# Kernel tuning notes

Hardware: AMD Instinct MI355X
Metric: run time of the kernel (lower is better)

The kernel has to match this reference:

```python
import jax, jax.numpy as jnp
import numpy as np

B, W, WIN_IN = 8, 2048, 1024
D, NH, DFF, L, KS = 512, 8, 2048, 4, 4
NGENES, G = 20000, 2048


def _ln(x, g, b, eps=1e-5):
    m = jnp.mean(x, -1, keepdims=True)
    v = jnp.var(x, -1, keepdims=True)
    return (x - m) * jax.lax.rsqrt(v + eps) * g + b


def _mha(q_in, kv_in, qkv_w, qkv_b, out_w, out_b, nh):
    d = q_in.shape[-1]
    hd = d // nh
    wq, wk, wv = qkv_w[:d], qkv_w[d:2 * d], qkv_w[2 * d:]
    bq, bk, bv = qkv_b[:d], qkv_b[d:2 * d], qkv_b[2 * d:]
    q = (q_in @ wq.T + bq).reshape(q_in.shape[0], q_in.shape[1], nh, hd)
    k = (kv_in @ wk.T + bk).reshape(kv_in.shape[0], kv_in.shape[1], nh, hd)
    v = (kv_in @ wv.T + bv).reshape(kv_in.shape[0], kv_in.shape[1], nh, hd)
    scores = jnp.einsum('bqhd,bkhd->bhqk', q, k) / jnp.sqrt(jnp.asarray(hd, q.dtype))
    a = jax.nn.softmax(scores, axis=-1)
    o = jnp.einsum('bhqk,bkhd->bqhd', a, v).reshape(q_in.shape[0], q_in.shape[1], d)
    return o @ out_w.T + out_b


def _posenc(S, d, dtype):
    pos = jnp.arange(S, dtype=jnp.float32)[:, None]
    div = jnp.exp(jnp.arange(0, d, 2, dtype=jnp.float32) * (-np.log(10000.0) / d))
    pe = jnp.zeros((S, d), jnp.float32)
    pe = pe.at[:, 0::2].set(jnp.sin(pos * div)).at[:, 1::2].set(jnp.cos(pos * div))
    return pe.astype(dtype)


def setup_inputs():
    key = jax.random.key(0)
    ks_ = jax.random.split(key, 12)

    def n(k, shape, s=0.02):
        return jax.random.normal(k, shape, jnp.float32) * s

    return dict(
        windows=jax.random.normal(ks_[0], (B, W, WIN_IN), jnp.float32),
        gene_ids=jax.random.randint(ks_[1], (G,), 0, NGENES),
        W_window=n(ks_[2], (D, WIN_IN)),
        enc_qkv_w=n(ks_[3], (L, 3 * D, D)),
        enc_qkv_b=jnp.zeros((L, 3 * D), jnp.float32),
        enc_out_w=n(ks_[4], (L, D, D)),
        enc_out_b=jnp.zeros((L, D), jnp.float32),
        enc_ln1_g=jnp.ones((L, D), jnp.float32),
        enc_ln1_b=jnp.zeros((L, D), jnp.float32),
        enc_ln2_g=jnp.ones((L, D), jnp.float32),
        enc_ln2_b=jnp.zeros((L, D), jnp.float32),
        enc_ff1_w=n(ks_[5], (L, DFF, D)),
        enc_ff1_b=jnp.zeros((L, DFF), jnp.float32),
        enc_ff2_w=n(ks_[6], (L, D, DFF)),
        enc_ff2_b=jnp.zeros((L, D), jnp.float32),
        gene_embed=n(ks_[7], (NGENES, D), 1.0),
        ca_qkv_w=n(ks_[8], (3 * D, D)),
        ca_qkv_b=jnp.zeros((3 * D,), jnp.float32),
        ca_out_w=n(ks_[9], (D, D)),
        ca_out_b=jnp.zeros((D,), jnp.float32),
        ro_ln_g=jnp.ones((D,), jnp.float32),
        ro_ln_b=jnp.zeros((D,), jnp.float32),
        ro_w=n(ks_[10], (1, D)),
        ro_b=jnp.zeros((1,), jnp.float32),
    )


def reference(windows, gene_ids, W_window, enc_qkv_w, enc_qkv_b, enc_out_w,
              enc_out_b, enc_ln1_g, enc_ln1_b, enc_ln2_g, enc_ln2_b,
              enc_ff1_w, enc_ff1_b, enc_ff2_w, enc_ff2_b, gene_embed,
              ca_qkv_w, ca_qkv_b, ca_out_w, ca_out_b, ro_ln_g, ro_ln_b,
              ro_w, ro_b):
    # proj_window (Linear, no bias; dropout inactive in eval)
    x = windows @ W_window.T                          # [B, W, D]
    Bn, Wn, _ = x.shape
    # AvgPool1d(kernel=stride=KS) along the window axis
    x = x.reshape(Bn, Wn // KS, KS, D).mean(axis=2)   # [B, S, D]
    S = x.shape[1]
    x = x + _posenc(S, D, x.dtype)[None]
    # pre-LN TransformerEncoder, relu FFN, no final norm
    for i in range(L):
        h = _ln(x, enc_ln1_g[i], enc_ln1_b[i])
        x = x + _mha(h, h, enc_qkv_w[i], enc_qkv_b[i], enc_out_w[i], enc_out_b[i], NH)
        h = _ln(x, enc_ln2_g[i], enc_ln2_b[i])
        x = x + (jax.nn.relu(h @ enc_ff1_w[i].T + enc_ff1_b[i]) @ enc_ff2_w[i].T + enc_ff2_b[i])
    # gene queries -> cross attention over encoded windows
    q = jnp.broadcast_to(gene_embed[gene_ids][None], (Bn, gene_ids.shape[0], D))
    z = _mha(q, x, ca_qkv_w, ca_qkv_b, ca_out_w, ca_out_b, NH)   # [B, G, D]
    pred = (_ln(z, ro_ln_g, ro_ln_b) @ ro_w.T + ro_b)[..., 0]    # [B, G]
    return pred, z
```

## Files before the change

### kernel.cpp

```cpp
#include <hip/hip_runtime.h>
#include <math.h>


typedef __attribute__((ext_vector_type(8))) short short8v;
typedef __attribute__((ext_vector_type(4))) float float4v;
typedef const __attribute__((address_space(1))) void* gas_t;
typedef __attribute__((address_space(3))) void* las_t;

__device__ inline unsigned short f2bf(float f) {
    unsigned int u = __builtin_bit_cast(unsigned int, f);
    return (unsigned short)((u + 0x7fffu + ((u >> 16) & 1u)) >> 16);
}

__device__ inline unsigned cvt_pk_bf16(float lo, float hi) {
    unsigned r;
    asm("v_cvt_pk_bf16_f32 %0, %1, %2" : "=v"(r) : "v"(lo), "v"(hi));
    return r;
}

__global__ __launch_bounds__(256) void cvt_k(const float* __restrict__ src,
                                             unsigned short* __restrict__ dst, int n4)
{
    int i = blockIdx.x * 256 + threadIdx.x;
    if (i >= n4) return;
    float4 v = ((const float4*)src)[i];
    ushort4 o;
    o.x = f2bf(v.x); o.y = f2bf(v.y); o.z = f2bf(v.z); o.w = f2bf(v.w);
    ((ushort4*)dst)[i] = o;
}

__global__ __launch_bounds__(256) void pool_windows_k(const float* __restrict__ win,
                                                      unsigned short* __restrict__ pw)
{
    int idx = blockIdx.x * 256 + threadIdx.x;
    int n = idx >> 8, c4 = (idx & 255) << 2;
    const float* base = win + (size_t)n * 4096 + c4;
    float4 a = *(const float4*)(base);
    float4 b2 = *(const float4*)(base + 1024);
    float4 c = *(const float4*)(base + 2048);
    float4 d = *(const float4*)(base + 3072);
    ushort4 r;
    r.x = f2bf((a.x + b2.x + c.x + d.x) * 0.25f);
    r.y = f2bf((a.y + b2.y + c.y + d.y) * 0.25f);
    r.z = f2bf((a.z + b2.z + c.z + d.z) * 0.25f);
    r.w = f2bf((a.w + b2.w + c.w + d.w) * 0.25f);
    ((ushort4*)pw)[idx] = r;
}

template<int BM, bool BIAS, bool BROW, bool RES, bool RELU, bool POSENC, bool O32, bool O16>
__global__ __launch_bounds__(256) void gemm_bf16_k(
    const unsigned short* __restrict__ A, const unsigned short* __restrict__ Bw,
    const float* __restrict__ bias, const float* __restrict__ Res,
    float* __restrict__ C32, unsigned short* __restrict__ C16,
    int M, int N, int K)
{
    constexpr int WC   = (BM == 128) ? 2 : 4;
    constexpr int NSTEP = 128 / WC;
    constexpr int MFR  = 4;
    constexpr int NFR  = NSTEP / 16;
    __shared__ __align__(16) unsigned short As[2][BM * 32];
    __shared__ __align__(16) unsigned short Bs[2][128 * 32];
    const int tid = threadIdx.x;
    const int lane = tid & 63;
    const int m0 = blockIdx.x * BM, n0 = blockIdx.y * 128;
    const int wr = (BM == 128) ? (tid >> 7) : 0;
    const int wc = (tid >> 6) & (WC - 1);
    const unsigned short* gA0 = A + (size_t)(m0 + (tid >> 2)) * K + (tid & 3) * 8;
    const unsigned short* gA1 = A + (size_t)(m0 + (tid >> 2) + 64) * K + (tid & 3) * 8;
    const unsigned short* gB0 = Bw + (size_t)(n0 + (tid >> 2)) * K + (tid & 3) * 8;
    const unsigned short* gB1 = Bw + (size_t)(n0 + (tid >> 2) + 64) * K + (tid & 3) * 8;
    const int r = lane & 15, g = lane >> 4;
    const int aoff = (64 * wr + r) * 32 + g * 8;
    const int boff = (NSTEP * wc + r) * 32 + g * 8;

    auto stage = [&](int bi, int k0) {
        __builtin_amdgcn_global_load_lds((gas_t)(gA0 + k0), (las_t)(&As[bi][tid * 8]), 16, 0, 0);
        if constexpr (BM == 128)
            __builtin_amdgcn_global_load_lds((gas_t)(gA1 + k0), (las_t)(&As[bi][(tid + 256) * 8]), 16, 0, 0);
        __builtin_amdgcn_global_load_lds((gas_t)(gB0 + k0), (las_t)(&Bs[bi][tid * 8]), 16, 0, 0);
        __builtin_amdgcn_global_load_lds((gas_t)(gB1 + k0), (las_t)(&Bs[bi][(tid + 256) * 8]), 16, 0, 0);
    };

    float4v acc[MFR][NFR];
    float4v z4 = {0.f, 0.f, 0.f, 0.f};
    #pragma unroll
    for (int i = 0; i < MFR; ++i)
        #pragma unroll
        for (int j = 0; j < NFR; ++j) acc[i][j] = z4;

    stage(0, 0);
    int buf = 0;
    for (int k0 = 0; k0 < K; k0 += 32) {
        __syncthreads();
        if (k0 + 32 < K) stage(buf ^ 1, k0 + 32);
        short8v a[MFR], b[NFR];
        #pragma unroll
        for (int mi = 0; mi < MFR; ++mi) a[mi] = *(const short8v*)&As[buf][aoff + mi * (16 * 32)];
        #pragma unroll
        for (int ni = 0; ni < NFR; ++ni) b[ni] = *(const short8v*)&Bs[buf][boff + ni * (16 * 32)];
        #pragma unroll
        for (int mi = 0; mi < MFR; ++mi)
            #pragma unroll
            for (int ni = 0; ni < NFR; ++ni)
                acc[mi][ni] = __builtin_amdgcn_mfma_f32_16x16x32_bf16(a[mi], b[ni], acc[mi][ni], 0, 0, 0);
        buf ^= 1;
    }

    #pragma unroll
    for (int mi = 0; mi < MFR; ++mi) {
        #pragma unroll
        for (int ni = 0; ni < NFR; ++ni) {
            const int row0 = m0 + 64 * wr + 16 * mi + g * 4;
            const int col  = n0 + NSTEP * wc + 16 * ni + r;
            float bv = (BIAS && !BROW) ? bias[col] : 0.f;
            float fr = 0.f;
            if (POSENC) fr = __expf((float)(col & ~1) * -0.01798894600f);
            #pragma unroll
            for (int q = 0; q < 4; ++q) {
                const int row = row0 + q;
                float v = acc[mi][ni][q] + bv;
                if (BIAS && BROW) v += bias[row];
                if (POSENC) {
                    float ang = (float)(row & 511) * fr;
                    v += (col & 1) ? __cosf(ang) : __sinf(ang);
                }
                if (RES) v += Res[(size_t)row * N + col];
                if (RELU) v = fmaxf(v, 0.0f);
                if (O32) C32[(size_t)row * N + col] = v;
                if (O16) C16[(size_t)row * N + col] = f2bf(v);
            }
        }
    }
}

template<bool SPLIT>
__global__ __launch_bounds__(256) void flashc_k(
    const unsigned short* __restrict__ Qp, long long q_bs, int q_rs,
    const unsigned short* __restrict__ Kp, long long k_bs, int k_rs,
    const unsigned short* __restrict__ Vtp, long long v_hs, long long v_bs, int v_rs,
    unsigned short* __restrict__ Op, long long o_bs, int o_rs,
    unsigned short* __restrict__ opart, float2* __restrict__ Ml,
    int nsplit, int nc)
{
    constexpr float C1 = 0.18033688011112042f;
    __shared__ __align__(16) unsigned short Kb[2][64 * 64];
    __shared__ __align__(16) unsigned short Vb[2][64 * 64];
    __shared__ __align__(16) unsigned short Ps[64 * 64];
    const int qt = blockIdx.x, h = blockIdx.y, z = blockIdx.z;
    const int b = z / nsplit, s = z - b * nsplit;
    const unsigned short* Q  = Qp  + (size_t)b * q_bs + (size_t)h * 64;
    const unsigned short* Kg = Kp  + (size_t)b * k_bs + (size_t)h * 64 + (size_t)(s * nc * 64) * k_rs;
    const unsigned short* Vg = Vtp + (size_t)h * v_hs + (size_t)b * v_bs + (size_t)(s * nc) * 64;
    const int q0 = qt * 64;
    const int tid = threadIdx.x, lane = tid & 63, w = tid >> 6;
    const int r = lane & 15, g = lane >> 4;
    const int sw8 = (r & 7) * 8;
    const int cA = (g * 8) ^ sw8;
    const int cB = ((g + 4) * 8) ^ sw8;
    const int prow = (16 * w + r) * 64;

    const unsigned short* qrow = Q + (size_t)(q0 + 16 * w + r) * q_rs + g * 8;
    short8v qf0 = *(const short8v*)(qrow);
    short8v qf1 = *(const short8v*)(qrow + 32);

    const int r0 = tid >> 3, cc = tid & 7;
    const int srcc = (cc ^ (r0 & 7)) * 8;
    auto stage = [&](int bi, int c) {
        const unsigned short* kc_ = Kg + (size_t)c * 64 * k_rs;
        const unsigned short* vc_ = Vg + (size_t)c * 64;
        __builtin_amdgcn_global_load_lds((gas_t)(kc_ + (size_t)r0 * k_rs + srcc),
                                         (las_t)(&Kb[bi][tid * 8]), 16, 0, 0);
        __builtin_amdgcn_global_load_lds((gas_t)(kc_ + (size_t)(r0 + 32) * k_rs + srcc),
                                         (las_t)(&Kb[bi][(tid + 256) * 8]), 16, 0, 0);
        __builtin_amdgcn_global_load_lds((gas_t)(vc_ + (size_t)r0 * v_rs + srcc),
                                         (las_t)(&Vb[bi][tid * 8]), 16, 0, 0);
        __builtin_amdgcn_global_load_lds((gas_t)(vc_ + (size_t)(r0 + 32) * v_rs + srcc),
                                         (las_t)(&Vb[bi][(tid + 256) * 8]), 16, 0, 0);
    };

    float4v acc_o[4];
    float4v z4 = {0.f, 0.f, 0.f, 0.f};
    #pragma unroll
    for (int dt = 0; dt < 4; ++dt) acc_o[dt] = z4;
    float m_own = -INFINITY, l_own = 0.f;

    stage(0, 0);
    __syncthreads();
    int buf = 0;

    for (int c = 0; c < nc; ++c) {
        if (c + 1 < nc) stage(buf ^ 1, c + 1);
        const unsigned short* KL = Kb[buf];
        const unsigned short* VL = Vb[buf];

        __builtin_amdgcn_s_setprio(1);
        float4v accs[4];
        #pragma unroll
        for (int t = 0; t < 4; ++t) {
            accs[t] = z4;
            const unsigned short* krow = KL + (16 * t + r) * 64;
            short8v kf0 = *(const short8v*)(krow + cA);
            short8v kf1 = *(const short8v*)(krow + cB);
            accs[t] = __builtin_amdgcn_mfma_f32_16x16x32_bf16(kf0, qf0, accs[t], 0, 0, 0);
            accs[t] = __builtin_amdgcn_mfma_f32_16x16x32_bf16(kf1, qf1, accs[t], 0, 0, 0);
        }
        __builtin_amdgcn_s_setprio(0);

        float m0_ = fmaxf(fmaxf(accs[0][0], accs[0][1]), fmaxf(accs[0][2], accs[0][3]));
        float m1_ = fmaxf(fmaxf(accs[1][0], accs[1][1]), fmaxf(accs[1][2], accs[1][3]));
        float m2_ = fmaxf(fmaxf(accs[2][0], accs[2][1]), fmaxf(accs[2][2], accs[2][3]));
        float m3_ = fmaxf(fmaxf(accs[3][0], accs[3][1]), fmaxf(accs[3][2], accs[3][3]));
        float sm = fmaxf(fmaxf(m0_, m1_), fmaxf(m2_, m3_));
        sm = fmaxf(sm, __shfl_xor(sm, 16));
        sm = fmaxf(sm, __shfl_xor(sm, 32));

        if (__any(sm > m_own + 64.f)) {
            float mn = fmaxf(m_own, sm);
            float alpha = __builtin_amdgcn_exp2f((m_own - mn) * C1);
            m_own = mn;
            float a0_ = __shfl(alpha, g * 4 + 0);
            float a1_ = __shfl(alpha, g * 4 + 1);
            float a2_ = __shfl(alpha, g * 4 + 2);
            float a3_ = __shfl(alpha, g * 4 + 3);
            #pragma unroll
            for (int dt = 0; dt < 4; ++dt) {
                acc_o[dt][0] *= a0_; acc_o[dt][1] *= a1_;
                acc_o[dt][2] *= a2_; acc_o[dt][3] *= a3_;
            }
            l_own *= alpha;
        }

        const float m2c = m_own * C1;
        float p[4][4];
        float rsum = 0.f;
        #pragma unroll
        for (int t = 0; t < 4; ++t)
            #pragma unroll
            for (int j = 0; j < 4; ++j) {
                float pv = __builtin_amdgcn_exp2f(__builtin_fmaf(accs[t][j], C1, -m2c));
                p[t][j] = pv; rsum += pv;
            }
        rsum += __shfl_xor(rsum, 16);
        rsum += __shfl_xor(rsum, 32);
        l_own += rsum;

        #pragma unroll
        for (int t = 0; t < 4; ++t) {
            uint2 uu;
            uu.x = cvt_pk_bf16(p[t][0], p[t][1]);
            uu.y = cvt_pk_bf16(p[t][2], p[t][3]);
            int pc = (((2 * t + (g >> 1)) * 8) ^ sw8) + (g & 1) * 4;
            *(uint2*)&Ps[prow + pc] = uu;
        }

        __builtin_amdgcn_s_setprio(1);
        short8v pf0 = *(const short8v*)&Ps[prow + cA];
        short8v pf1 = *(const short8v*)&Ps[prow + cB];
        #pragma unroll
        for (int dt = 0; dt < 4; ++dt) {
            const unsigned short* vrow = VL + (16 * dt + r) * 64;
            short8v vf0 = *(const short8v*)(vrow + cA);
            short8v vf1 = *(const short8v*)(vrow + cB);
            acc_o[dt] = __builtin_amdgcn_mfma_f32_16x16x32_bf16(pf0, vf0, acc_o[dt], 0, 0, 0);
            acc_o[dt] = __builtin_amdgcn_mfma_f32_16x16x32_bf16(pf1, vf1, acc_o[dt], 0, 0, 0);
        }
        __builtin_amdgcn_s_setprio(0);

        __syncthreads();
        buf ^= 1;
    }

    float il0 = 1.f / __shfl(l_own, g * 4 + 0);
    float il1 = 1.f / __shfl(l_own, g * 4 + 1);
    float il2 = 1.f / __shfl(l_own, g * 4 + 2);
    float il3 = 1.f / __shfl(l_own, g * 4 + 3);
    if (SPLIT) {
        unsigned short* Ob = opart + ((size_t)(s * 4096 + b * 512)) * 512 + h * 64;
        #pragma unroll
        for (int dt = 0; dt < 4; ++dt) {
            Ob[(size_t)(q0 + 16 * w + g * 4 + 0) * 512 + 16 * dt + r] = f2bf(acc_o[dt][0] * il0);
            Ob[(size_t)(q0 + 16 * w + g * 4 + 1) * 512 + 16 * dt + r] = f2bf(acc_o[dt][1] * il1);
            Ob[(size_t)(q0 + 16 * w + g * 4 + 2) * 512 + 16 * dt + r] = f2bf(acc_o[dt][2] * il2);
            Ob[(size_t)(q0 + 16 * w + g * 4 + 3) * 512 + 16 * dt + r] = f2bf(acc_o[dt][3] * il3);
        }
        if (g == 0)
            Ml[((size_t)(s * 8 + b) * 8 + h) * 512 + q0 + 16 * w + r] = make_float2(m_own, l_own);
    } else {
        unsigned short* O = Op + (size_t)b * o_bs + (size_t)h * 64;
        #pragma unroll
        for (int dt = 0; dt < 4; ++dt) {
            O[(size_t)(q0 + 16 * w + g * 4 + 0) * o_rs + 16 * dt + r] = f2bf(acc_o[dt][0] * il0);
            O[(size_t)(q0 + 16 * w + g * 4 + 1) * o_rs + 16 * dt + r] = f2bf(acc_o[dt][1] * il1);
            O[(size_t)(q0 + 16 * w + g * 4 + 2) * o_rs + 16 * dt + r] = f2bf(acc_o[dt][2] * il2);
            O[(size_t)(q0 + 16 * w + g * 4 + 3) * o_rs + 16 * dt + r] = f2bf(acc_o[dt][3] * il3);
        }
    }
}

template<int NS>
__global__ __launch_bounds__(256) void combine_k(const unsigned short* __restrict__ opart,
                                                 const float2* __restrict__ Ml,
                                                 unsigned short* __restrict__ Oo)
{
    constexpr float C1 = 0.18033688011112042f;
    const int row = blockIdx.x;
    const int b = row >> 9, srow = row & 511;
    const int tid = threadIdx.x;
    const int h = tid >> 5, t = tid & 31;
    float2 ml[NS];
    float m = -INFINITY;
    #pragma unroll
    for (int s = 0; s < NS; ++s) {
        ml[s] = Ml[((size_t)(s * 8 + b) * 8 + h) * 512 + srow];
        m = fmaxf(m, ml[s].x);
    }
    float wgt[NS];
    float wsum = 0.f;
    #pragma unroll
    for (int s = 0; s < NS; ++s) {
        wgt[s] = __builtin_amdgcn_exp2f((ml[s].x - m) * C1) * ml[s].y;
        wsum += wgt[s];
    }
    float inv = 1.f / wsum;
    const int col = h * 64 + t * 2;
    float acc0 = 0.f, acc1 = 0.f;
    #pragma unroll
    for (int s = 0; s < NS; ++s) {
        unsigned u = *(const unsigned*)&opart[((size_t)s * 4096 + row) * 512 + col];
        acc0 += wgt[s] * __builtin_bit_cast(float, (u & 0xffffu) << 16);
        acc1 += wgt[s] * __builtin_bit_cast(float, (u >> 16) << 16);
    }
    *(unsigned*)&Oo[(size_t)row * 512 + col] = cvt_pk_bf16(acc0 * inv, acc1 * inv);
}

__global__ __launch_bounds__(64) void ln_k(const float* __restrict__ X, unsigned short* __restrict__ Y,
                                           const float* __restrict__ g, const float* __restrict__ bt)
{
    int row = blockIdx.x, lane = threadIdx.x;
    const float* x = X + (size_t)row * 512;
    int c0 = lane * 4, c1 = 256 + lane * 4;
    float4 a0 = *(const float4*)&x[c0];
    float4 a1 = *(const float4*)&x[c1];
    float s  = a0.x + a0.y + a0.z + a0.w + a1.x + a1.y + a1.z + a1.w;
    float ss = a0.x * a0.x + a0.y * a0.y + a0.z * a0.z + a0.w * a0.w
             + a1.x * a1.x + a1.y * a1.y + a1.z * a1.z + a1.w * a1.w;
    #pragma unroll
    for (int off = 1; off < 64; off <<= 1) { s += __shfl_xor(s, off); ss += __shfl_xor(ss, off); }
    float mean = s * (1.f / 512.f);
    float var  = ss * (1.f / 512.f) - mean * mean;
    float rs = rsqrtf(var + 1e-5f);
    float4 g0 = *(const float4*)&g[c0], g1 = *(const float4*)&g[c1];
    float4 b0 = *(const float4*)&bt[c0], b1 = *(const float4*)&bt[c1];
    unsigned short* y = Y + (size_t)row * 512;
    ushort4 o0, o1;
    o0.x = f2bf((a0.x - mean) * rs * g0.x + b0.x);  o0.y = f2bf((a0.y - mean) * rs * g0.y + b0.y);
    o0.z = f2bf((a0.z - mean) * rs * g0.z + b0.z);  o0.w = f2bf((a0.w - mean) * rs * g0.w + b0.w);
    o1.x = f2bf((a1.x - mean) * rs * g1.x + b1.x);  o1.y = f2bf((a1.y - mean) * rs * g1.y + b1.y);
    o1.z = f2bf((a1.z - mean) * rs * g1.z + b1.z);  o1.w = f2bf((a1.w - mean) * rs * g1.w + b1.w);
    *(ushort4*)&y[c0] = o0;
    *(ushort4*)&y[c1] = o1;
}

__global__ __launch_bounds__(128) void gather_k(const float* __restrict__ ge, const int* __restrict__ ids,
                                                unsigned short* __restrict__ out)
{
    int gi = blockIdx.x, t = threadIdx.x;
    int id = ids[gi];
    float4 v = *(const float4*)&ge[(size_t)id * 512 + t * 4];
    ushort4 o;
    o.x = f2bf(v.x); o.y = f2bf(v.y); o.z = f2bf(v.z); o.w = f2bf(v.w);
    *(ushort4*)&out[(size_t)gi * 512 + t * 4] = o;
}

__global__ __launch_bounds__(64) void readout_k(const float* __restrict__ Z,
                                                const float* __restrict__ g, const float* __restrict__ bt,
                                                const float* __restrict__ rw, const float* __restrict__ rb,
                                                float* __restrict__ pred)
{
    int row = blockIdx.x, lane = threadIdx.x;
    const float* zr = Z + (size_t)row * 512;
    int c0 = lane * 4, c1 = 256 + lane * 4;
    float4 a0 = *(const float4*)&zr[c0];
    float4 a1 = *(const float4*)&zr[c1];
    float s  = a0.x + a0.y + a0.z + a0.w + a1.x + a1.y + a1.z + a1.w;
    float ss = a0.x * a0.x + a0.y * a0.y + a0.z * a0.z + a0.w * a0.w
             + a1.x * a1.x + a1.y * a1.y + a1.z * a1.z + a1.w * a1.w;
    #pragma unroll
    for (int off = 1; off < 64; off <<= 1) { s += __shfl_xor(s, off); ss += __shfl_xor(ss, off); }
    float mean = s * (1.f / 512.f);
    float var  = ss * (1.f / 512.f) - mean * mean;
    float rs = rsqrtf(var + 1e-5f);
    float4 g0 = *(const float4*)&g[c0], g1 = *(const float4*)&g[c1];
    float4 b0 = *(const float4*)&bt[c0], b1 = *(const float4*)&bt[c1];
    float4 w0 = *(const float4*)&rw[c0], w1 = *(const float4*)&rw[c1];
    float acc = 0.f;
    acc += ((a0.x - mean) * rs * g0.x + b0.x) * w0.x;
    acc += ((a0.y - mean) * rs * g0.y + b0.y) * w0.y;
    acc += ((a0.z - mean) * rs * g0.z + b0.z) * w0.z;
    acc += ((a0.w - mean) * rs * g0.w + b0.w) * w0.w;
    acc += ((a1.x - mean) * rs * g1.x + b1.x) * w1.x;
    acc += ((a1.y - mean) * rs * g1.y + b1.y) * w1.y;
    acc += ((a1.z - mean) * rs * g1.z + b1.z) * w1.z;
    acc += ((a1.w - mean) * rs * g1.w + b1.w) * w1.w;
    #pragma unroll
    for (int off = 1; off < 64; off <<= 1) acc += __shfl_xor(acc, off);
    if (lane == 0) pred[row] = acc + rb[0];
}

extern "C" void kernel_launch(void* const* d_in, const int* in_sizes, int n_in,
                              void* d_out, int out_size, void* d_ws, size_t ws_size,
                              hipStream_t stream)
{
    (void)in_sizes; (void)n_in; (void)out_size; (void)ws_size;
    const float* windows    = (const float*)d_in[0];
    const int*   gene_ids   = (const int*)  d_in[1];
    const float* W_window   = (const float*)d_in[2];
    const float* enc_qkv_w  = (const float*)d_in[3];
    const float* enc_qkv_b  = (const float*)d_in[4];
    const float* enc_out_w  = (const float*)d_in[5];
    const float* enc_out_b  = (const float*)d_in[6];
    const float* enc_ln1_g  = (const float*)d_in[7];
    const float* enc_ln1_b  = (const float*)d_in[8];
    const float* enc_ln2_g  = (const float*)d_in[9];
    const float* enc_ln2_b  = (const float*)d_in[10];
    const float* enc_ff1_w  = (const float*)d_in[11];
    const float* enc_ff1_b  = (const float*)d_in[12];
    const float* enc_ff2_w  = (const float*)d_in[13];
    const float* enc_ff2_b  = (const float*)d_in[14];
    const float* gene_embed = (const float*)d_in[15];
    const float* ca_qkv_w   = (const float*)d_in[16];
    const float* ca_qkv_b   = (const float*)d_in[17];
    const float* ca_out_w   = (const float*)d_in[18];
    const float* ca_out_b   = (const float*)d_in[19];
    const float* ro_ln_g    = (const float*)d_in[20];
    const float* ro_ln_b    = (const float*)d_in[21];
    const float* ro_w       = (const float*)d_in[22];
    const float* ro_b       = (const float*)d_in[23];

    float* pred = (float*)d_out;
    float* z    = pred + (size_t)8 * 2048;

    char* wp = (char*)d_ws;
    float* x = (float*)wp;                       wp += (size_t)4096 * 512 * 4;
    unsigned short* x16   = (unsigned short*)wp; wp += (size_t)4096 * 512 * 2;
    unsigned short* h16   = (unsigned short*)wp; wp += (size_t)4096 * 512 * 2;
    unsigned short* qkv16 = (unsigned short*)wp; wp += (size_t)4096 * 1536 * 2;
    unsigned short* ao16  = (unsigned short*)wp; wp += (size_t)4096 * 512 * 2;
    unsigned short* big16 = (unsigned short*)wp; wp += (size_t)16384 * 512 * 2;
    unsigned short* vt16  = (unsigned short*)wp; wp += (size_t)512 * 4096 * 2;
    unsigned short* wW16     = (unsigned short*)wp; wp += (size_t)512 * 1024 * 2;
    unsigned short* wqkv16   = (unsigned short*)wp; wp += (size_t)4 * 1536 * 512 * 2;
    unsigned short* wout16   = (unsigned short*)wp; wp += (size_t)4 * 512 * 512 * 2;
    unsigned short* wff116   = (unsigned short*)wp; wp += (size_t)4 * 2048 * 512 * 2;
    unsigned short* wff216   = (unsigned short*)wp; wp += (size_t)4 * 512 * 2048 * 2;
    unsigned short* wcaqkv16 = (unsigned short*)wp; wp += (size_t)1536 * 512 * 2;
    unsigned short* wcaout16 = (unsigned short*)wp; wp += (size_t)512 * 512 * 2;
    unsigned short* pw16    = big16;
    unsigned short* ff116   = big16;
    unsigned short* oc16    = big16;
    unsigned short* opart16 = big16;
    float2* mlbuf = (float2*)(big16 + (size_t)2 * 4096 * 512);
    unsigned short* ge16  = qkv16;
    unsigned short* qg16  = qkv16 + (size_t)2048 * 512;
    unsigned short* kc16  = qkv16 + (size_t)2 * 2048 * 512;

    auto cvt = [&](const float* s, unsigned short* d, int n) {
        cvt_k<<<(n / 4 + 255) / 256, 256, 0, stream>>>(s, d, n / 4);
    };
    cvt(W_window,  wW16,     512 * 1024);
    cvt(enc_qkv_w, wqkv16,   4 * 1536 * 512);
    cvt(enc_out_w, wout16,   4 * 512 * 512);
    cvt(enc_ff1_w, wff116,   4 * 2048 * 512);
    cvt(enc_ff2_w, wff216,   4 * 512 * 2048);
    cvt(ca_qkv_w,  wcaqkv16, 1536 * 512);
    cvt(ca_out_w,  wcaout16, 512 * 512);

    pool_windows_k<<<4096, 256, 0, stream>>>(windows, pw16);
    gemm_bf16_k<64, false, false, false, false, true, true, false><<<dim3(64, 4), 256, 0, stream>>>(
        pw16, wW16, nullptr, nullptr, x, nullptr, 4096, 512, 1024);

    for (int l = 0; l < 4; ++l) {
        const unsigned short* wl = wqkv16 + (size_t)l * 1536 * 512;
        ln_k<<<4096, 64, 0, stream>>>(x, h16, enc_ln1_g + l * 512, enc_ln1_b + l * 512);
        gemm_bf16_k<128, true, false, false, false, false, false, true><<<dim3(32, 8), 256, 0, stream>>>(
            h16, wl, enc_qkv_b + l * 1536, nullptr, nullptr, qkv16, 4096, 1024, 512);
        gemm_bf16_k<64, true, true, false, false, false, false, true><<<dim3(8, 32), 256, 0, stream>>>(
            wl + (size_t)1024 * 512, h16, enc_qkv_b + l * 1536 + 1024, nullptr,
            nullptr, vt16, 512, 4096, 512);
        flashc_k<true><<<dim3(8, 8, 16), 256, 0, stream>>>(
            qkv16, (long long)512 * 1024, 1024,
            qkv16 + 512, (long long)512 * 1024, 1024,
            vt16, (long long)64 * 4096, 512LL, 4096,
            nullptr, 0LL, 0,
            opart16, mlbuf, 2, 4);
        combine_k<2><<<4096, 256, 0, stream>>>(opart16, mlbuf, ao16);
        gemm_bf16_k<64, true, false, true, false, false, true, false><<<dim3(64, 4), 256, 0, stream>>>(
            ao16, wout16 + (size_t)l * 512 * 512, enc_out_b + l * 512, x, x, nullptr, 4096, 512, 512);
        ln_k<<<4096, 64, 0, stream>>>(x, h16, enc_ln2_g + l * 512, enc_ln2_b + l * 512);
        gemm_bf16_k<128, true, false, false, true, false, false, true><<<dim3(32, 16), 256, 0, stream>>>(
            h16, wff116 + (size_t)l * 2048 * 512, enc_ff1_b + l * 2048, nullptr,
            nullptr, ff116, 4096, 2048, 512);
        if (l == 3)
            gemm_bf16_k<64, true, false, true, false, false, true, true><<<dim3(64, 4), 256, 0, stream>>>(
                ff116, wff216 + (size_t)l * 512 * 2048, enc_ff2_b + l * 512, x, x, x16, 4096, 512, 2048);
        else
            gemm_bf16_k<64, true, false, true, false, false, true, false><<<dim3(64, 4), 256, 0, stream>>>(
                ff116, wff216 + (size_t)l * 512 * 2048, enc_ff2_b + l * 512, x, x, nullptr, 4096, 512, 2048);
    }

    gather_k<<<2048, 128, 0, stream>>>(gene_embed, gene_ids, ge16);
    gemm_bf16_k<64, true, false, false, false, false, false, true><<<dim3(32, 4), 256, 0, stream>>>(
        ge16, wcaqkv16, ca_qkv_b, nullptr, nullptr, qg16, 2048, 512, 512);
    gemm_bf16_k<64, true, false, false, false, false, false, true><<<dim3(64, 4), 256, 0, stream>>>(
        x16, wcaqkv16 + (size_t)512 * 512, ca_qkv_b + 512, nullptr, nullptr, kc16, 4096, 512, 512);
    gemm_bf16_k<64, true, true, false, false, false, false, true><<<dim3(8, 32), 256, 0, stream>>>(
        wcaqkv16 + (size_t)1024 * 512, x16, ca_qkv_b + 1024, nullptr, nullptr, vt16, 512, 4096, 512);
    flashc_k<false><<<dim3(32, 8, 8), 256, 0, stream>>>(
        qg16, 0LL, 512,
        kc16, (long long)512 * 512, 512,
        vt16, (long long)64 * 4096, 512LL, 4096,
        oc16, (long long)2048 * 512, 512,
        nullptr, nullptr, 1, 8);
    gemm_bf16_k<128, true, false, false, false, false, true, false><<<dim3(128, 4), 256, 0, stream>>>(
        oc16, wcaout16, ca_out_b, nullptr, z, nullptr, 16384, 512, 512);

    readout_k<<<16384, 64, 0, stream>>>(z, ro_ln_g, ro_ln_b, ro_w, ro_b, pred);
}
```

Before: 602.2 us.

## Deepen GEMM K-tile, XOR-swizzle LDS, and overlap loads with explicit vmcnt waits

The GEMM main loop is restructured. BM=64 tiles now use a 64-wide K slice, LDS columns are XOR-swizzled to avoid bank conflicts, and the single __syncthreads is replaced by explicit s_waitcnt vmcnt plus raw s_barrier, so the next stage's global-to-LDS loads stay in flight across the barrier. This is meant to cut barrier and LDS conflict stalls and improve load/compute overlap. In exchange, BM=64 uses more LDS and the code depends on the hand-counted vmcnt matching the number of outstanding loads.

```diff
diff --git a/kernel.cpp b/kernel.cpp
--- a/kernel.cpp
+++ b/kernel.cpp
@@ -54,31 +54,44 @@
     float* __restrict__ C32, unsigned short* __restrict__ C16,
     int M, int N, int K)
 {
+    constexpr int BK   = (BM == 128) ? 32 : 64;
+    constexpr int CPR  = BK / 8;
     constexpr int WC   = (BM == 128) ? 2 : 4;
     constexpr int NSTEP = 128 / WC;
     constexpr int MFR  = 4;
     constexpr int NFR  = NSTEP / 16;
-    __shared__ __align__(16) unsigned short As[2][BM * 32];
-    __shared__ __align__(16) unsigned short Bs[2][128 * 32];
+    constexpr int LPTA = BM * BK / 2048;
+    constexpr int LPTB = 128 * BK / 2048;
+    constexpr int LPT  = LPTA + LPTB;
+    __shared__ __align__(16) unsigned short As[2][BM * BK];
+    __shared__ __align__(16) unsigned short Bs[2][128 * BK];
     const int tid = threadIdx.x;
     const int lane = tid & 63;
     const int m0 = blockIdx.x * BM, n0 = blockIdx.y * 128;
     const int wr = (BM == 128) ? (tid >> 7) : 0;
     const int wc = (tid >> 6) & (WC - 1);
-    const unsigned short* gA0 = A + (size_t)(m0 + (tid >> 2)) * K + (tid & 3) * 8;
-    const unsigned short* gA1 = A + (size_t)(m0 + (tid >> 2) + 64) * K + (tid & 3) * 8;
-    const unsigned short* gB0 = Bw + (size_t)(n0 + (tid >> 2)) * K + (tid & 3) * 8;
-    const unsigned short* gB1 = Bw + (size_t)(n0 + (tid >> 2) + 64) * K + (tid & 3) * 8;
     const int r = lane & 15, g = lane >> 4;
-    const int aoff = (64 * wr + r) * 32 + g * 8;
-    const int boff = (NSTEP * wc + r) * 32 + g * 8;
+
+    const unsigned short* gA[LPTA];
+    const unsigned short* gB[LPTB];
+    #pragma unroll
+    for (int j = 0; j < LPTA; ++j) {
+        int c = tid + j * 256, row = c / CPR, cc = c % CPR;
+        gA[j] = A + (size_t)(m0 + row) * K + ((cc ^ (row & (CPR - 1))) * 8);
+    }
+    #pragma unroll
+    for (int j = 0; j < LPTB; ++j) {
+        int c = tid + j * 256, row = c / CPR, cc = c % CPR;
+        gB[j] = Bw + (size_t)(n0 + row) * K + ((cc ^ (row & (CPR - 1))) * 8);
+    }
 
     auto stage = [&](int bi, int k0) {
-        __builtin_amdgcn_global_load_lds((gas_t)(gA0 + k0), (las_t)(&As[bi][tid * 8]), 16, 0, 0);
-        if constexpr (BM == 128)
-            __builtin_amdgcn_global_load_lds((gas_t)(gA1 + k0), (las_t)(&As[bi][(tid + 256) * 8]), 16, 0, 0);
-        __builtin_amdgcn_global_load_lds((gas_t)(gB0 + k0), (las_t)(&Bs[bi][tid * 8]), 16, 0, 0);
-        __builtin_amdgcn_global_load_lds((gas_t)(gB1 + k0), (las_t)(&Bs[bi][(tid + 256) * 8]), 16, 0, 0);
+        #pragma unroll
+        for (int j = 0; j < LPTA; ++j)
+            __builtin_amdgcn_global_load_lds((gas_t)(gA[j] + k0), (las_t)(&As[bi][(tid + j * 256) * 8]), 16, 0, 0);
+        #pragma unroll
+        for (int j = 0; j < LPTB; ++j)
+            __builtin_amdgcn_global_load_lds((gas_t)(gB[j] + k0), (las_t)(&Bs[bi][(tid + j * 256) * 8]), 16, 0, 0);
     };
 
     float4v acc[MFR][NFR];
@@ -90,19 +103,35 @@
 
     stage(0, 0);
     int buf = 0;
-    for (int k0 = 0; k0 < K; k0 += 32) {
-        __syncthreads();
-        if (k0 + 32 < K) stage(buf ^ 1, k0 + 32);
-        short8v a[MFR], b[NFR];
-        #pragma unroll
-        for (int mi = 0; mi < MFR; ++mi) a[mi] = *(const short8v*)&As[buf][aoff + mi * (16 * 32)];
-        #pragma unroll
-        for (int ni = 0; ni < NFR; ++ni) b[ni] = *(const short8v*)&Bs[buf][boff + ni * (16 * 32)];
-        #pragma unroll
-        for (int mi = 0; mi < MFR; ++mi)
+    for (int k0 = 0; k0 < K; k0 += BK) {
+        if (k0 + BK < K) {
+            stage(buf ^ 1, k0 + BK);
+            if constexpr (LPT == 4) asm volatile("s_waitcnt vmcnt(4)" ::: "memory");
+            else                    asm volatile("s_waitcnt vmcnt(6)" ::: "memory");
+        } else {
+            asm volatile("s_waitcnt vmcnt(0)" ::: "memory");
+        }
+        __builtin_amdgcn_sched_barrier(0);
+        __builtin_amdgcn_s_barrier();
+        __builtin_amdgcn_sched_barrier(0);
+        #pragma unroll
+        for (int kk = 0; kk < BK / 32; ++kk) {
+            const int cx = ((kk * 4 + g) ^ (r & (CPR - 1))) * 8;
+            short8v a[MFR], b[NFR];
+            #pragma unroll
+            for (int mi = 0; mi < MFR; ++mi)
+                a[mi] = *(const short8v*)&As[buf][(64 * wr + 16 * mi + r) * BK + cx];
             #pragma unroll
             for (int ni = 0; ni < NFR; ++ni)
-                acc[mi][ni] = __builtin_amdgcn_mfma_f32_16x16x32_bf16(a[mi], b[ni], acc[mi][ni], 0, 0, 0);
+                b[ni] = *(const short8v*)&Bs[buf][(NSTEP * wc + 16 * ni + r) * BK + cx];
+            #pragma unroll
+            for (int mi = 0; mi < MFR; ++mi)
+                #pragma unroll
+                for (int ni = 0; ni < NFR; ++ni)
+                    acc[mi][ni] = __builtin_amdgcn_mfma_f32_16x16x32_bf16(a[mi], b[ni], acc[mi][ni], 0, 0, 0);
+        }
+        __builtin_amdgcn_sched_barrier(0);
+        __builtin_amdgcn_s_barrier();
         buf ^= 1;
     }
 
```

Result: faster. 579.3 us (-3.8%).
